# Kernel tuning notes

Hardware: AMD Instinct MI355X
Metric: run time of the kernel (lower is better)

## Reference

```python
import jax, jax.numpy as jnp
import numpy as np

N_ATOMS = 100000
N_EDGES = 400000
N_MOLS = 4000
D_ATOM = 64
D_MSG = 128
N_STEPS = 3
N_MSG_HID = 1
D_RO = 256
N_RO_HID = 2
D_OUT = 1


def setup_inputs() -> dict:
    key = jax.random.key(0)
    ks = jax.random.split(key, 20)

    def w(k, shape, fan_in):
        return jax.random.normal(k, shape, dtype=jnp.float32) / np.sqrt(fan_in)

    return {
        "atom_states": jax.random.normal(ks[0], (N_ATOMS, D_ATOM), dtype=jnp.float32),
        "edge_src": jax.random.randint(ks[1], (N_EDGES,), 0, N_ATOMS, dtype=jnp.int32),
        "edge_dst": jax.random.randint(ks[2], (N_EDGES,), 0, N_ATOMS, dtype=jnp.int32),
        "mol_ids": jnp.sort(jax.random.randint(ks[3], (N_ATOMS,), 0, N_MOLS, dtype=jnp.int32)),
        "ms_W_in": w(ks[4], (N_STEPS, 2 * D_ATOM, D_MSG), 2 * D_ATOM),
        "ms_b_in": w(ks[5], (N_STEPS, D_MSG), 2 * D_ATOM),
        "ms_W_h": w(ks[6], (N_STEPS, N_MSG_HID, D_MSG, D_MSG), D_MSG),
        "ms_b_h": w(ks[7], (N_STEPS, N_MSG_HID, D_MSG), D_MSG),
        "ms_W_out": w(ks[8], (N_STEPS, D_MSG, D_ATOM), D_MSG),
        "ms_b_out": w(ks[9], (N_STEPS, D_ATOM), D_MSG),
        "ro_W_in": w(ks[10], (D_ATOM, D_RO), D_ATOM),
        "ro_b_in": w(ks[11], (D_RO,), D_ATOM),
        "ro_W_h": w(ks[12], (N_RO_HID, D_RO, D_RO), D_RO),
        "ro_b_h": w(ks[13], (N_RO_HID, D_RO), D_RO),
        "ro_W_out": w(ks[14], (D_RO, D_OUT), D_RO),
        "ro_b_out": w(ks[15], (D_OUT,), D_RO),
    }


def reference(atom_states, edge_src, edge_dst, mol_ids,
              ms_W_in, ms_b_in, ms_W_h, ms_b_h, ms_W_out, ms_b_out,
              ro_W_in, ro_b_in, ro_W_h, ro_b_h, ro_W_out, ro_b_out):
    n_atoms = atom_states.shape[0]
    states = atom_states
    # Message passing: per edge, message = MLP_step(concat(state[src], state[dst]));
    # new atom state = sum of messages over the atom's edges (aggregated at src).
    for s in range(ms_W_in.shape[0]):
        msg = jnp.concatenate([states[edge_src], states[edge_dst]], axis=-1)  # [E, 2*D]
        h = jax.nn.relu(msg @ ms_W_in[s] + ms_b_in[s])                        # [E, D_MSG]
        for l in range(ms_W_h.shape[1]):
            h = jax.nn.relu(h @ ms_W_h[s, l] + ms_b_h[s, l])
        m = jax.nn.relu(h @ ms_W_out[s] + ms_b_out[s])                        # [E, D]
        states = jax.ops.segment_sum(m, edge_src, num_segments=n_atoms)       # [N, D]
    # Readout: molecule representation = sum of its atom states, then MLP.
    mol_repr = jax.ops.segment_sum(states, mol_ids, num_segments=N_MOLS)      # [M, D]
    out = jax.nn.relu(mol_repr @ ro_W_in + ro_b_in)
    for l in range(ro_W_h.shape[0]):
        out = jax.nn.relu(out @ ro_W_h[l] + ro_b_h[l])
    return out @ ro_W_out + ro_b_out                                          # [M, D_OUT]
```

## Files before the change

### kernel.cpp

```cpp
#include <hip/hip_runtime.h>
#include <hip/hip_bf16.h>

#define K_N_ATOMS 100000
#define K_N_EDGES 400000
#define K_N_MOLS  4000

typedef __attribute__((ext_vector_type(8))) short bf16x8;
typedef __attribute__((ext_vector_type(4))) float f32x4;

__device__ __forceinline__ unsigned short f2bf(float x) {
  union { __hip_bfloat16 b; unsigned short u; } c;
  c.b = __float2bfloat16(x);
  return c.u;
}

__device__ __forceinline__ float bf2f(unsigned short u) {
  union { float f; unsigned u; } c;
  c.u = ((unsigned)u) << 16;
  return c.f;
}

__device__ __forceinline__ unsigned pk2(float a, float b) {
  union { __hip_bfloat162 h; unsigned u; } c;
  c.h = __float22bfloat162_rn(make_float2(a, b));
  return c.u;
}

__device__ __forceinline__ bf16x8 pack8(float4 x, float4 y) {
  union { bf16x8 v; unsigned u[4]; } r;
  r.u[0] = pk2(x.x, x.y); r.u[1] = pk2(x.z, x.w);
  r.u[2] = pk2(y.x, y.y); r.u[3] = pk2(y.z, y.w);
  return r.v;
}

__device__ __forceinline__ float relu(float x) { return fmaxf(x, 0.f); }

__device__ __forceinline__ bf16x8 addrelu8(bf16x8 a, bf16x8 b) {
  union { bf16x8 v; unsigned short s[8]; } ua, ub;
  ua.v = a; ub.v = b;
  union { bf16x8 v; unsigned u[4]; } r;
#pragma unroll
  for (int q = 0; q < 4; ++q) {
    float x0 = relu(bf2f(ua.s[2 * q]) + bf2f(ub.s[2 * q]));
    float x1 = relu(bf2f(ua.s[2 * q + 1]) + bf2f(ub.s[2 * q + 1]));
    r.u[q] = pk2(x0, x1);
  }
  return r.v;
}

__global__ void prep_w(const float* __restrict__ Win, const float* __restrict__ Wh,
                       const float* __restrict__ Wout, unsigned short* __restrict__ wf) {
  int s = blockIdx.y;
  int flat = (blockIdx.x * 256 + threadIdx.x) * 4;
  if (flat < 16384) {
    const float* W = Win + s * 16384;
    unsigned short* dst = wf + s * 40960;
    int k = flat >> 7, j = flat & 127;
    float4 w4 = *(const float4*)(W + flat);
    float wv[4] = {w4.x, w4.y, w4.z, w4.w};
#pragma unroll
    for (int c = 0; c < 4; ++c) {
      int jj = j + c, kk = k;
      if (k >= 64) { kk = k - 64; jj += 128; }
      int jt = jj >> 4, ks = kk >> 5, ln = (jj & 15) + 16 * ((kk >> 3) & 3), i = kk & 7;
      dst[((jt * 2 + ks) * 64 + ln) * 8 + i] = f2bf(wv[c]);
    }
  } else if (flat < 32768) {
    const float* W = Wh + s * 16384;
    unsigned short* dst = wf + s * 40960 + 16384;
    int local = flat - 16384;
    int k = local >> 7, j = local & 127;
    float4 w4 = *(const float4*)(W + local);
    float wv[4] = {w4.x, w4.y, w4.z, w4.w};
    int ks = k >> 5, kr = (k >> 3) & 3, i = k & 7;
#pragma unroll
    for (int c = 0; c < 4; ++c) {
      int jj = j + c;
      int jt = jj >> 4, ln = (jj & 15) + 16 * kr;
      dst[((jt * 4 + ks) * 64 + ln) * 8 + i] = f2bf(wv[c]);
    }
  } else {
    const float* W = Wout + s * 8192;
    unsigned short* dst = wf + s * 40960 + 32768;
    int local = flat - 32768;
    int k = local >> 6, j = local & 63;
    float4 w4 = *(const float4*)(W + local);
    float wv[4] = {w4.x, w4.y, w4.z, w4.w};
    int ks = k >> 5, kr = (k >> 3) & 3, i = k & 7;
#pragma unroll
    for (int c = 0; c < 4; ++c) {
      int jj = j + c;
      int jt = jj >> 4, ln = (jj & 15) + 16 * kr;
      dst[((jt * 4 + ks) * 64 + ln) * 8 + i] = f2bf(wv[c]);
    }
  }
}

__global__ void k_hist(const int* __restrict__ esrc, int* __restrict__ cnt) {
  int t = blockIdx.x * 256 + threadIdx.x;
  if (t < K_N_EDGES) atomicAdd(&cnt[esrc[t]], 1);
}

__global__ void k_blocksum(const int* __restrict__ cnt, int* __restrict__ partial) {
  __shared__ int red[256];
  int i = blockIdx.x * 256 + threadIdx.x;
  red[threadIdx.x] = (i < K_N_ATOMS) ? cnt[i] : 0;
  __syncthreads();
  for (int off = 128; off; off >>= 1) {
    if (threadIdx.x < off) red[threadIdx.x] += red[threadIdx.x + off];
    __syncthreads();
  }
  if (!threadIdx.x) partial[blockIdx.x] = red[0];
}

__global__ void k_scanpart2(int* __restrict__ partial, int nb) {
  __shared__ int sh[512];
  int tid = threadIdx.x;
  int v = (tid < nb) ? partial[tid] : 0;
  sh[tid] = v;
  __syncthreads();
  for (int off = 1; off < 512; off <<= 1) {
    int t = (tid >= off) ? sh[tid - off] : 0;
    __syncthreads();
    sh[tid] += t;
    __syncthreads();
  }
  if (tid < nb) partial[tid] = sh[tid] - v;
}

__global__ void k_scanfinal_bounds(const int* __restrict__ cnt, const int* __restrict__ poffs,
                                   int* __restrict__ start, int* __restrict__ cur,
                                   const int* __restrict__ mol_ids, int* __restrict__ mstart) {
  __shared__ int sh[256];
  int tid = threadIdx.x;
  int i = blockIdx.x * 256 + tid;
  int v = (i < K_N_ATOMS) ? cnt[i] : 0;
  sh[tid] = v;
  __syncthreads();
  for (int off = 1; off < 256; off <<= 1) {
    int t = (tid >= off) ? sh[tid - off] : 0;
    __syncthreads();
    sh[tid] += t;
    __syncthreads();
  }
  int ex = sh[tid] - v + poffs[blockIdx.x];
  if (i < K_N_ATOMS) { start[i] = ex; cur[i] = ex; }
  if (i == K_N_ATOMS - 1) start[K_N_ATOMS] = ex + v;

  if (i < K_N_ATOMS) {
    int id = mol_ids[i];
    int prev = (i == 0) ? -1 : mol_ids[i - 1];
    for (int m = prev + 1; m <= id; ++m) mstart[m] = i;
    if (i == K_N_ATOMS - 1)
      for (int m = id + 1; m <= K_N_MOLS; ++m) mstart[m] = K_N_ATOMS;
  }
}

__global__ void k_scatter(const int* __restrict__ esrc, const int* __restrict__ edst,
                          int* __restrict__ cur, int2* __restrict__ ep) {
  int t = blockIdx.x * 256 + threadIdx.x;
  if (t < K_N_EDGES) {
    int s = esrc[t];
    int p = atomicAdd(&cur[s], 1);
    ep[p] = make_int2(s, edst[t]);
  }
}

__global__ __launch_bounds__(256, 4) void fg_gemm0(
    const float* __restrict__ st_in, unsigned short* __restrict__ Fb,
    unsigned short* __restrict__ Gb,
    const unsigned short* __restrict__ wfg, const float* __restrict__ bin) {
  const int tid = threadIdx.x;
  const int wave = tid >> 6, lane = tid & 63, lo = lane & 15, h = lane >> 4;
  const int atom0 = (blockIdx.x * 4 + wave) * 16;
  const int a = atom0 + lo;
  const int ac = (a < K_N_ATOMS) ? a : (K_N_ATOMS - 1);

  const float* row = st_in + (size_t)ac * 64 + h * 8;
  bf16x8 b0 = pack8(*(const float4*)row, *(const float4*)(row + 4));
  bf16x8 b1 = pack8(*(const float4*)(row + 32), *(const float4*)(row + 36));

#pragma unroll
  for (int jt = 0; jt < 16; ++jt) {
    f32x4 acc;
    if (jt < 8) acc = *(const f32x4*)(bin + jt * 16 + h * 4);
    else { acc[0] = 0.f; acc[1] = 0.f; acc[2] = 0.f; acc[3] = 0.f; }
    bf16x8 a0 = *(const bf16x8*)(wfg + ((jt * 2 + 0) * 64 + lane) * 8);
    bf16x8 a1 = *(const bf16x8*)(wfg + ((jt * 2 + 1) * 64 + lane) * 8);
    acc = __builtin_amdgcn_mfma_f32_16x16x32_bf16(a0, b0, acc, 0, 0, 0);
    acc = __builtin_amdgcn_mfma_f32_16x16x32_bf16(a1, b1, acc, 0, 0, 0);
    if (a < K_N_ATOMS) {
      unsigned short* dst = (jt < 8) ? (Fb + (size_t)a * 128 + jt * 16 + h * 4)
                                     : (Gb + (size_t)a * 128 + (jt - 8) * 16 + h * 4);
      *(uint2*)dst = make_uint2(pk2(acc[0], acc[1]), pk2(acc[2], acc[3]));
    }
  }
}

__global__ __launch_bounds__(256, 4) void agg_fg(
    const unsigned short* __restrict__ m_buf, const int* __restrict__ start,
    unsigned short* __restrict__ Fb, unsigned short* __restrict__ Gb,
    const unsigned short* __restrict__ wfg, const float* __restrict__ bin) {
  const int tid = threadIdx.x;
  const int wave = tid >> 6, lane = tid & 63, lo = lane & 15, h = lane >> 4;
  const int atom0 = (blockIdx.x * 4 + wave) * 16;
  const int a = atom0 + lo;

  int s = 0, e = 0;
  if (a < K_N_ATOMS) { s = start[a]; e = start[a + 1]; }

  float acc[16];
#pragma unroll
  for (int q = 0; q < 16; ++q) acc[q] = 0.f;
  int r = s;
  for (; r + 2 <= e; r += 2) {
    const unsigned short* p0 = m_buf + (size_t)r * 64 + h * 8;
    const unsigned short* p1 = m_buf + (size_t)(r + 1) * 64 + h * 8;
    union { bf16x8 v; unsigned short w[8]; } u0, u1, u2, u3;
    u0.v = *(const bf16x8*)(p0);
    u1.v = *(const bf16x8*)(p0 + 32);
    u2.v = *(const bf16x8*)(p1);
    u3.v = *(const bf16x8*)(p1 + 32);
#pragma unroll
    for (int q = 0; q < 8; ++q) {
      acc[q] += bf2f(u0.w[q]) + bf2f(u2.w[q]);
      acc[8 + q] += bf2f(u1.w[q]) + bf2f(u3.w[q]);
    }
  }
  if (r < e) {
    const unsigned short* p = m_buf + (size_t)r * 64 + h * 8;
    union { bf16x8 v; unsigned short w[8]; } u0, u1;
    u0.v = *(const bf16x8*)(p);
    u1.v = *(const bf16x8*)(p + 32);
#pragma unroll
    for (int q = 0; q < 8; ++q) { acc[q] += bf2f(u0.w[q]); acc[8 + q] += bf2f(u1.w[q]); }
  }
  union { bf16x8 v; unsigned u[4]; } c0, c1;
#pragma unroll
  for (int q = 0; q < 4; ++q) {
    c0.u[q] = pk2(acc[2 * q], acc[2 * q + 1]);
    c1.u[q] = pk2(acc[8 + 2 * q], acc[8 + 2 * q + 1]);
  }
  bf16x8 b0 = c0.v, b1 = c1.v;

#pragma unroll
  for (int jt = 0; jt < 16; ++jt) {
    f32x4 d;
    if (jt < 8) d = *(const f32x4*)(bin + jt * 16 + h * 4);
    else { d[0] = 0.f; d[1] = 0.f; d[2] = 0.f; d[3] = 0.f; }
    bf16x8 a0 = *(const bf16x8*)(wfg + ((jt * 2 + 0) * 64 + lane) * 8);
    bf16x8 a1 = *(const bf16x8*)(wfg + ((jt * 2 + 1) * 64 + lane) * 8);
    d = __builtin_amdgcn_mfma_f32_16x16x32_bf16(a0, b0, d, 0, 0, 0);
    d = __builtin_amdgcn_mfma_f32_16x16x32_bf16(a1, b1, d, 0, 0, 0);
    if (a < K_N_ATOMS) {
      unsigned short* dst = (jt < 8) ? (Fb + (size_t)a * 128 + jt * 16 + h * 4)
                                     : (Gb + (size_t)a * 128 + (jt - 8) * 16 + h * 4);
      *(uint2*)dst = make_uint2(pk2(d[0], d[1]), pk2(d[2], d[3]));
    }
  }
}

__device__ __forceinline__ void layer128_2(const unsigned short* wf,
                                           const float* __restrict__ bias,
                                           bf16x8 (&bfr)[2][4], unsigned (&p)[2][8][2],
                                           int lane, int h) {
#pragma unroll
  for (int jt = 0; jt < 8; ++jt) {
    f32x4 bv = *(const f32x4*)(bias + jt * 16 + h * 4);
    f32x4 a0 = bv, a1 = bv;
#pragma unroll
    for (int ks = 0; ks < 4; ++ks) {
      bf16x8 a = *(const bf16x8*)(wf + ((jt * 4 + ks) * 64 + lane) * 8);
      a0 = __builtin_amdgcn_mfma_f32_16x16x32_bf16(a, bfr[0][ks], a0, 0, 0, 0);
      a1 = __builtin_amdgcn_mfma_f32_16x16x32_bf16(a, bfr[1][ks], a1, 0, 0, 0);
    }
    p[0][jt][0] = pk2(relu(a0[0]), relu(a0[1])); p[0][jt][1] = pk2(relu(a0[2]), relu(a0[3]));
    p[1][jt][0] = pk2(relu(a1[0]), relu(a1[1])); p[1][jt][1] = pk2(relu(a1[2]), relu(a1[3]));
  }
}

__device__ __forceinline__ void transpose_p2(const unsigned (&p)[2][8][2], bf16x8 (&bfr)[2][4],
                                             int lo, int h) {
  const int hsel = (h & 1) * 2;
#pragma unroll
  for (int et = 0; et < 2; ++et) {
#pragma unroll
    for (int ks = 0; ks < 4; ++ks) {
      union { unsigned u[4]; bf16x8 v; } cv;
#pragma unroll
      for (int w = 0; w < 4; ++w) {
        int srcLane = lo + 16 * (hsel + (w >> 1));
        unsigned d0 = (unsigned)__shfl((int)p[et][2 * ks][w & 1], srcLane, 64);
        unsigned d1 = (unsigned)__shfl((int)p[et][2 * ks + 1][w & 1], srcLane, 64);
        cv.u[w] = (h < 2) ? d0 : d1;
      }
      bfr[et][ks] = cv.v;
    }
  }
}

__global__ __launch_bounds__(512, 4) void edge_msg4(
    const unsigned short* __restrict__ Fb, const unsigned short* __restrict__ Gb,
    unsigned short* __restrict__ m_buf,
    const int2* __restrict__ ep, const unsigned short* __restrict__ wf23,
    const float* __restrict__ b2, const float* __restrict__ b3) {
  __shared__ unsigned short wl[24576];
  const int tid = threadIdx.x;
  const int wave = tid >> 6, lane = tid & 63, lo = lane & 15, h = lane >> 4;
  const int ebase = blockIdx.x * 256 + wave * 32;

  int srcs[2], dsts[2];
  unsigned vmask = 0;
#pragma unroll
  for (int et = 0; et < 2; ++et) {
    int e = ebase + et * 16 + lo;
    if (e < K_N_EDGES) vmask |= 1u << et;
    int ec = (e < K_N_EDGES) ? e : (K_N_EDGES - 1);
    int2 pr = ep[ec];
    srcs[et] = pr.x;
    dsts[et] = pr.y;
  }
  __builtin_amdgcn_sched_barrier(0);

  bf16x8 wreg[6];
#pragma unroll
  for (int i = 0; i < 6; ++i)
    wreg[i] = ((const bf16x8*)wf23)[i * 512 + tid];
  __builtin_amdgcn_sched_barrier(0);

  bf16x8 fr[2][4], gr[2][4];
#pragma unroll
  for (int et = 0; et < 2; ++et) {
    const unsigned short* pf = Fb + (size_t)srcs[et] * 128 + h * 8;
    const unsigned short* pg = Gb + (size_t)dsts[et] * 128 + h * 8;
#pragma unroll
    for (int ks = 0; ks < 4; ++ks) {
      fr[et][ks] = *(const bf16x8*)(pf + ks * 32);
      gr[et][ks] = *(const bf16x8*)(pg + ks * 32);
    }
  }
  __builtin_amdgcn_sched_barrier(0);

#pragma unroll
  for (int i = 0; i < 6; ++i)
    ((bf16x8*)wl)[i * 512 + tid] = wreg[i];
  __syncthreads();

  bf16x8 bfr[2][4];
#pragma unroll
  for (int et = 0; et < 2; ++et)
#pragma unroll
    for (int ks = 0; ks < 4; ++ks)
      bfr[et][ks] = addrelu8(fr[et][ks], gr[et][ks]);

  unsigned p[2][8][2];
  layer128_2(wl, b2, bfr, p, lane, h);
  transpose_p2(p, bfr, lo, h);

  const unsigned short* w3 = wl + 16384;
#pragma unroll
  for (int jt = 0; jt < 4; ++jt) {
    f32x4 bv = *(const f32x4*)(b3 + jt * 16 + h * 4);
    f32x4 a0 = bv, a1 = bv;
#pragma unroll
    for (int ks = 0; ks < 4; ++ks) {
      bf16x8 a = *(const bf16x8*)(w3 + ((jt * 4 + ks) * 64 + lane) * 8);
      a0 = __builtin_amdgcn_mfma_f32_16x16x32_bf16(a, bfr[0][ks], a0, 0, 0, 0);
      a1 = __builtin_amdgcn_mfma_f32_16x16x32_bf16(a, bfr[1][ks], a1, 0, 0, 0);
    }
    f32x4 accs[2] = {a0, a1};
#pragma unroll
    for (int et = 0; et < 2; ++et) {
      if (vmask & (1u << et)) {
        int e = ebase + et * 16 + lo;
        *(uint2*)(m_buf + (size_t)e * 64 + jt * 16 + h * 4) =
            make_uint2(pk2(relu(accs[et][0]), relu(accs[et][1])),
                       pk2(relu(accs[et][2]), relu(accs[et][3])));
      }
    }
  }
}

__global__ __launch_bounds__(256) void mol_msum(
    const unsigned short* __restrict__ m_buf, const int* __restrict__ start,
    const int* __restrict__ mstart, float* __restrict__ mol) {
  int wv = (blockIdx.x * 256 + threadIdx.x) >> 6;
  int lane = threadIdx.x & 63;
  if (wv >= K_N_MOLS) return;
  int sub = lane & 7, rg = lane >> 3;
  int s = start[mstart[wv]], e = start[mstart[wv + 1]];
  float acc[8] = {0.f, 0.f, 0.f, 0.f, 0.f, 0.f, 0.f, 0.f};
  for (int r = s + rg; r < e; r += 8) {
    union { bf16x8 v; unsigned short w[8]; } u;
    u.v = *(const bf16x8*)(m_buf + (size_t)r * 64 + sub * 8);
#pragma unroll
    for (int q = 0; q < 8; ++q) acc[q] += bf2f(u.w[q]);
  }
#pragma unroll
  for (int off = 8; off <= 32; off <<= 1) {
#pragma unroll
    for (int q = 0; q < 8; ++q) acc[q] += __shfl_xor(acc[q], off, 64);
  }
  if (rg == 0) {
    float* p = mol + (size_t)wv * 64 + sub * 8;
    *(float4*)(p) = make_float4(acc[0], acc[1], acc[2], acc[3]);
    *(float4*)(p + 4) = make_float4(acc[4], acc[5], acc[6], acc[7]);
  }
}

__global__ __launch_bounds__(256) void ro_fused(
    const float* __restrict__ mol, const float* __restrict__ Win,
    const float* __restrict__ bin, const float* __restrict__ Wh,
    const float* __restrict__ bh, const float* __restrict__ Wout,
    const float* __restrict__ bout, float* __restrict__ out) {
  __shared__ float a[8][64];
  __shared__ float h0[8][260];
  __shared__ float h1[8][260];
  __shared__ float red[8][256];
  int m0 = blockIdx.x * 8;
  int t = threadIdx.x;
  for (int flat = t; flat < 512; flat += 256) {
    int m = flat >> 6, k = flat & 63;
    a[m][k] = mol[(size_t)(m0 + m) * 64 + k];
  }
  __syncthreads();
  const int j = t;
  float acc[8];
  {
    float b = bin[j];
#pragma unroll
    for (int m = 0; m < 8; ++m) acc[m] = b;
    for (int k = 0; k < 64; k += 4) {
      float w0 = Win[k * 256 + j], w1 = Win[(k + 1) * 256 + j];
      float w2 = Win[(k + 2) * 256 + j], w3 = Win[(k + 3) * 256 + j];
#pragma unroll
      for (int m = 0; m < 8; ++m) {
        float4 hv = *(const float4*)&a[m][k];
        acc[m] += hv.x * w0 + hv.y * w1 + hv.z * w2 + hv.w * w3;
      }
    }
#pragma unroll
    for (int m = 0; m < 8; ++m) h0[m][j] = relu(acc[m]);
  }
  __syncthreads();
  {
    float b = bh[j];
#pragma unroll
    for (int m = 0; m < 8; ++m) acc[m] = b;
    for (int k = 0; k < 256; k += 4) {
      float w0 = Wh[k * 256 + j], w1 = Wh[(k + 1) * 256 + j];
      float w2 = Wh[(k + 2) * 256 + j], w3 = Wh[(k + 3) * 256 + j];
#pragma unroll
      for (int m = 0; m < 8; ++m) {
        float4 hv = *(const float4*)&h0[m][k];
        acc[m] += hv.x * w0 + hv.y * w1 + hv.z * w2 + hv.w * w3;
      }
    }
#pragma unroll
    for (int m = 0; m < 8; ++m) h1[m][j] = relu(acc[m]);
  }
  __syncthreads();
  {
    float b = bh[256 + j];
#pragma unroll
    for (int m = 0; m < 8; ++m) acc[m] = b;
    for (int k = 0; k < 256; k += 4) {
      float w0 = Wh[65536 + k * 256 + j], w1 = Wh[65536 + (k + 1) * 256 + j];
      float w2 = Wh[65536 + (k + 2) * 256 + j], w3 = Wh[65536 + (k + 3) * 256 + j];
#pragma unroll
      for (int m = 0; m < 8; ++m) {
        float4 hv = *(const float4*)&h1[m][k];
        acc[m] += hv.x * w0 + hv.y * w1 + hv.z * w2 + hv.w * w3;
      }
    }
#pragma unroll
    for (int m = 0; m < 8; ++m) h0[m][j] = relu(acc[m]);
  }
  __syncthreads();
  {
    float wj = Wout[j];
#pragma unroll
    for (int m = 0; m < 8; ++m) red[m][j] = h0[m][j] * wj;
  }
  __syncthreads();
  for (int off = 128; off; off >>= 1) {
    if (j < off) {
#pragma unroll
      for (int m = 0; m < 8; ++m) red[m][j] += red[m][j + off];
    }
    __syncthreads();
  }
  if (j < 8) out[m0 + j] = red[j][0] + bout[0];
}

extern "C" void kernel_launch(void* const* d_in, const int* in_sizes, int n_in,
                              void* d_out, int out_size, void* d_ws, size_t ws_size,
                              hipStream_t stream) {
  const float* atom_states = (const float*)d_in[0];
  const int* esrc = (const int*)d_in[1];
  const int* edst = (const int*)d_in[2];
  const int* mol_ids = (const int*)d_in[3];
  const float* msWin = (const float*)d_in[4];
  const float* msbin = (const float*)d_in[5];
  const float* msWh = (const float*)d_in[6];
  const float* msbh = (const float*)d_in[7];
  const float* msWout = (const float*)d_in[8];
  const float* msbout = (const float*)d_in[9];
  const float* roWin = (const float*)d_in[10];
  const float* robin = (const float*)d_in[11];
  const float* roWh = (const float*)d_in[12];
  const float* robh = (const float*)d_in[13];
  const float* roWout = (const float*)d_in[14];
  const float* robout = (const float*)d_in[15];
  float* out = (float*)d_out;

  unsigned short* m_buf = (unsigned short*)d_ws;
  unsigned short* Fb = m_buf + (size_t)K_N_EDGES * 64;
  unsigned short* Gb = Fb + (size_t)K_N_ATOMS * 128;
  int2* ep = (int2*)(Gb + (size_t)K_N_ATOMS * 128);
  int* cnt = (int*)(ep + K_N_EDGES);
  int* start = cnt + K_N_ATOMS;
  int* cur = start + K_N_ATOMS + 1;
  int* partial = cur + K_N_ATOMS;
  unsigned short* wfb = (unsigned short*)(partial + 512);
  int* mstart = (int*)(wfb + 3 * 40960);
  float* mol = (float*)Fb;

  const int EG = (K_N_EDGES + 255) / 256;
  const int AG = (K_N_ATOMS + 255) / 256;
  const int AG16 = (K_N_ATOMS + 63) / 64;

  prep_w<<<dim3(40, 3), 256, 0, stream>>>(msWin, msWh, msWout, wfb);

  hipMemsetAsync(cnt, 0, K_N_ATOMS * sizeof(int), stream);
  k_hist<<<EG, 256, 0, stream>>>(esrc, cnt);
  k_blocksum<<<AG, 256, 0, stream>>>(cnt, partial);
  k_scanpart2<<<1, 512, 0, stream>>>(partial, AG);
  k_scanfinal_bounds<<<AG, 256, 0, stream>>>(cnt, partial, start, cur, mol_ids, mstart);
  k_scatter<<<EG, 256, 0, stream>>>(esrc, edst, cur, ep);

  fg_gemm0<<<AG16, 256, 0, stream>>>(atom_states, Fb, Gb, wfb, msbin);
  edge_msg4<<<EG, 512, 0, stream>>>(Fb, Gb, m_buf, ep, wfb + 16384, msbh, msbout);
  agg_fg<<<AG16, 256, 0, stream>>>(m_buf, start, Fb, Gb, wfb + 40960, msbin + 128);
  edge_msg4<<<EG, 512, 0, stream>>>(Fb, Gb, m_buf, ep, wfb + 40960 + 16384,
                                    msbh + 128, msbout + 64);
  agg_fg<<<AG16, 256, 0, stream>>>(m_buf, start, Fb, Gb, wfb + 81920, msbin + 256);
  edge_msg4<<<EG, 512, 0, stream>>>(Fb, Gb, m_buf, ep, wfb + 81920 + 16384,
                                    msbh + 256, msbout + 128);

  mol_msum<<<(K_N_MOLS * 64 + 255) / 256, 256, 0, stream>>>(m_buf, start, mstart, mol);
  ro_fused<<<K_N_MOLS / 8, 256, 0, stream>>>(mol, roWin, robin, roWh, robh,
                                             roWout, robout, out);
}
```

Before: 334.7 us.

## Process two edge tiles per block with software-pipelined gathers in edge MLP

The edge message kernel now handles two 256-edge tiles per block (782 blocks instead of 1563). The weight staging into LDS is amortised over both tiles. The gathers of F/G rows for the second tile are issued between the MFMA layers of the first tile to hide gather latency. This raises register pressure, which could hurt occupancy or cause spills under the 512x4 launch bounds, and halves the block count.

```diff
diff --git a/kernel.cpp b/kernel.cpp
--- a/kernel.cpp
+++ b/kernel.cpp
@@ -4,6 +4,7 @@
 #define K_N_ATOMS 100000
 #define K_N_EDGES 400000
 #define K_N_MOLS  4000
+#define K_NB      782
 
 typedef __attribute__((ext_vector_type(8))) short bf16x8;
 typedef __attribute__((ext_vector_type(4))) float f32x4;
@@ -299,7 +300,36 @@
   }
 }
 
-__global__ __launch_bounds__(512, 4) void edge_msg4(
+__device__ __forceinline__ void layer3_store(const unsigned short* w3,
+                                             const float* __restrict__ b3,
+                                             bf16x8 (&bfr)[2][4],
+                                             unsigned short* __restrict__ m_buf,
+                                             int ebase, unsigned vmask,
+                                             int lane, int lo, int h) {
+#pragma unroll
+  for (int jt = 0; jt < 4; ++jt) {
+    f32x4 bv = *(const f32x4*)(b3 + jt * 16 + h * 4);
+    f32x4 a0 = bv, a1 = bv;
+#pragma unroll
+    for (int ks = 0; ks < 4; ++ks) {
+      bf16x8 a = *(const bf16x8*)(w3 + ((jt * 4 + ks) * 64 + lane) * 8);
+      a0 = __builtin_amdgcn_mfma_f32_16x16x32_bf16(a, bfr[0][ks], a0, 0, 0, 0);
+      a1 = __builtin_amdgcn_mfma_f32_16x16x32_bf16(a, bfr[1][ks], a1, 0, 0, 0);
+    }
+    f32x4 accs[2] = {a0, a1};
+#pragma unroll
+    for (int et = 0; et < 2; ++et) {
+      if (vmask & (1u << et)) {
+        int e = ebase + et * 16 + lo;
+        *(uint2*)(m_buf + (size_t)e * 64 + jt * 16 + h * 4) =
+            make_uint2(pk2(relu(accs[et][0]), relu(accs[et][1])),
+                       pk2(relu(accs[et][2]), relu(accs[et][3])));
+      }
+    }
+  }
+}
+
+__global__ __launch_bounds__(512, 4) void edge_msg5(
     const unsigned short* __restrict__ Fb, const unsigned short* __restrict__ Gb,
     unsigned short* __restrict__ m_buf,
     const int2* __restrict__ ep, const unsigned short* __restrict__ wf23,
@@ -307,18 +337,26 @@
   __shared__ unsigned short wl[24576];
   const int tid = threadIdx.x;
   const int wave = tid >> 6, lane = tid & 63, lo = lane & 15, h = lane >> 4;
-  const int ebase = blockIdx.x * 256 + wave * 32;
-
-  int srcs[2], dsts[2];
-  unsigned vmask = 0;
+  const int eb0 = blockIdx.x * 256 + wave * 32;
+  const int eb1 = (K_NB + blockIdx.x) * 256 + wave * 32;
+
+  int srcs0[2], dsts0[2], srcs1[2], dsts1[2];
+  unsigned vm0 = 0, vm1 = 0;
 #pragma unroll
   for (int et = 0; et < 2; ++et) {
-    int e = ebase + et * 16 + lo;
-    if (e < K_N_EDGES) vmask |= 1u << et;
+    int e = eb0 + et * 16 + lo;
+    if (e < K_N_EDGES) vm0 |= 1u << et;
     int ec = (e < K_N_EDGES) ? e : (K_N_EDGES - 1);
     int2 pr = ep[ec];
-    srcs[et] = pr.x;
-    dsts[et] = pr.y;
+    srcs0[et] = pr.x; dsts0[et] = pr.y;
+  }
+#pragma unroll
+  for (int et = 0; et < 2; ++et) {
+    int e = eb1 + et * 16 + lo;
+    if (e < K_N_EDGES) vm1 |= 1u << et;
+    int ec = (e < K_N_EDGES) ? e : (K_N_EDGES - 1);
+    int2 pr = ep[ec];
+    srcs1[et] = pr.x; dsts1[et] = pr.y;
   }
   __builtin_amdgcn_sched_barrier(0);
 
@@ -331,8 +369,8 @@
   bf16x8 fr[2][4], gr[2][4];
 #pragma unroll
   for (int et = 0; et < 2; ++et) {
-    const unsigned short* pf = Fb + (size_t)srcs[et] * 128 + h * 8;
-    const unsigned short* pg = Gb + (size_t)dsts[et] * 128 + h * 8;
+    const unsigned short* pf = Fb + (size_t)srcs0[et] * 128 + h * 8;
+    const unsigned short* pg = Gb + (size_t)dsts0[et] * 128 + h * 8;
 #pragma unroll
     for (int ks = 0; ks < 4; ++ks) {
       fr[et][ks] = *(const bf16x8*)(pf + ks * 32);
@@ -346,39 +384,52 @@
     ((bf16x8*)wl)[i * 512 + tid] = wreg[i];
   __syncthreads();
 
+  const unsigned short* w3 = wl + 16384;
+
   bf16x8 bfr[2][4];
 #pragma unroll
   for (int et = 0; et < 2; ++et)
 #pragma unroll
     for (int ks = 0; ks < 4; ++ks)
       bfr[et][ks] = addrelu8(fr[et][ks], gr[et][ks]);
+  __builtin_amdgcn_sched_barrier(0);
+
+  bf16x8 fr1[2][4];
+#pragma unroll
+  for (int et = 0; et < 2; ++et) {
+    const unsigned short* pf = Fb + (size_t)srcs1[et] * 128 + h * 8;
+#pragma unroll
+    for (int ks = 0; ks < 4; ++ks)
+      fr1[et][ks] = *(const bf16x8*)(pf + ks * 32);
+  }
+  __builtin_amdgcn_sched_barrier(0);
 
   unsigned p[2][8][2];
   layer128_2(wl, b2, bfr, p, lane, h);
   transpose_p2(p, bfr, lo, h);
-
-  const unsigned short* w3 = wl + 16384;
-#pragma unroll
-  for (int jt = 0; jt < 4; ++jt) {
-    f32x4 bv = *(const f32x4*)(b3 + jt * 16 + h * 4);
-    f32x4 a0 = bv, a1 = bv;
-#pragma unroll
-    for (int ks = 0; ks < 4; ++ks) {
-      bf16x8 a = *(const bf16x8*)(w3 + ((jt * 4 + ks) * 64 + lane) * 8);
-      a0 = __builtin_amdgcn_mfma_f32_16x16x32_bf16(a, bfr[0][ks], a0, 0, 0, 0);
-      a1 = __builtin_amdgcn_mfma_f32_16x16x32_bf16(a, bfr[1][ks], a1, 0, 0, 0);
-    }
-    f32x4 accs[2] = {a0, a1};
-#pragma unroll
-    for (int et = 0; et < 2; ++et) {
-      if (vmask & (1u << et)) {
-        int e = ebase + et * 16 + lo;
-        *(uint2*)(m_buf + (size_t)e * 64 + jt * 16 + h * 4) =
-            make_uint2(pk2(relu(accs[et][0]), relu(accs[et][1])),
-                       pk2(relu(accs[et][2]), relu(accs[et][3])));
-      }
-    }
-  }
+  __builtin_amdgcn_sched_barrier(0);
+
+  bf16x8 gr1[2][4];
+#pragma unroll
+  for (int et = 0; et < 2; ++et) {
+    const unsigned short* pg = Gb + (size_t)dsts1[et] * 128 + h * 8;
+#pragma unroll
+    for (int ks = 0; ks < 4; ++ks)
+      gr1[et][ks] = *(const bf16x8*)(pg + ks * 32);
+  }
+  __builtin_amdgcn_sched_barrier(0);
+
+  layer3_store(w3, b3, bfr, m_buf, eb0, vm0, lane, lo, h);
+
+#pragma unroll
+  for (int et = 0; et < 2; ++et)
+#pragma unroll
+    for (int ks = 0; ks < 4; ++ks)
+      bfr[et][ks] = addrelu8(fr1[et][ks], gr1[et][ks]);
+
+  layer128_2(wl, b2, bfr, p, lane, h);
+  transpose_p2(p, bfr, lo, h);
+  layer3_store(w3, b3, bfr, m_buf, eb1, vm1, lane, lo, h);
 }
 
 __global__ __launch_bounds__(256) void mol_msum(
@@ -540,13 +591,13 @@
   k_scatter<<<EG, 256, 0, stream>>>(esrc, edst, cur, ep);
 
   fg_gemm0<<<AG16, 256, 0, stream>>>(atom_states, Fb, Gb, wfb, msbin);
-  edge_msg4<<<EG, 512, 0, stream>>>(Fb, Gb, m_buf, ep, wfb + 16384, msbh, msbout);
+  edge_msg5<<<K_NB, 512, 0, stream>>>(Fb, Gb, m_buf, ep, wfb + 16384, msbh, msbout);
   agg_fg<<<AG16, 256, 0, stream>>>(m_buf, start, Fb, Gb, wfb + 40960, msbin + 128);
-  edge_msg4<<<EG, 512, 0, stream>>>(Fb, Gb, m_buf, ep, wfb + 40960 + 16384,
-                                    msbh + 128, msbout + 64);
+  edge_msg5<<<K_NB, 512, 0, stream>>>(Fb, Gb, m_buf, ep, wfb + 40960 + 16384,
+                                      msbh + 128, msbout + 64);
   agg_fg<<<AG16, 256, 0, stream>>>(m_buf, start, Fb, Gb, wfb + 81920, msbin + 256);
-  edge_msg4<<<EG, 512, 0, stream>>>(Fb, Gb, m_buf, ep, wfb + 81920 + 16384,
-                                    msbh + 256, msbout + 128);
+  edge_msg5<<<K_NB, 512, 0, stream>>>(Fb, Gb, m_buf, ep, wfb + 81920 + 16384,
+                                      msbh + 256, msbout + 128);
 
   mol_msum<<<(K_N_MOLS * 64 + 255) / 256, 256, 0, stream>>>(m_buf, start, mstart, mol);
   ro_fused<<<K_N_MOLS / 8, 256, 0, stream>>>(mol, roWin, robin, roWh, robh,
```

Result: slower. 495.0 us (+47.9%).
